# Optimization experiments

Hardware: AMD Instinct MI355X
Metric: run time of the kernel (lower is better)

Reference implementation:

```python
import jax, jax.numpy as jnp
import numpy as np

H, E, K = 1024, 8, 2  # hidden_size, num_experts, top_k
B, S = 2, 4096


def setup_inputs() -> dict:
    key = jax.random.key(0)
    ks = jax.random.split(key, 5)
    s = 1.0 / np.sqrt(H)
    return {
        "x": jax.random.normal(ks[0], (B, S, H), dtype=jnp.float32),
        "ln_scale": jnp.ones((H,), jnp.float32),
        "ln_bias": jnp.zeros((H,), jnp.float32),
        "w1": (jax.random.normal(ks[1], (H, H), jnp.float32) * s),
        "b1": jnp.zeros((H,), jnp.float32),
        "w2": (jax.random.normal(ks[2], (H, E), jnp.float32) * s),
        "b2": jnp.zeros((E,), jnp.float32),
        "We": (jax.random.normal(ks[3], (E, H, H), jnp.float32) * s),
        "be": jnp.zeros((E, H), jnp.float32),
    }


def _layernorm(x, scale, bias, eps=1e-5):
    m = jnp.mean(x, axis=-1, keepdims=True)
    v = jnp.var(x, axis=-1, keepdims=True)
    return (x - m) * jax.lax.rsqrt(v + eps) * scale + bias


def reference(x, ln_scale, ln_bias, w1, b1, w2, b2, We, be):
    b, s, h = x.shape
    # --- router (BaseRouter): LN -> MLP -> softmax -> top-k -> renorm ---
    xn = _layernorm(x, ln_scale, ln_bias)
    hmid = jax.nn.relu(xn @ w1 + b1)
    logits = hmid @ w2 + b2                      # [B,S,E]
    probs = jax.nn.softmax(logits, axis=-1)
    topk_p, topk_i = jax.lax.top_k(probs, K)     # [B,S,K]
    topk_p = topk_p / jnp.sum(topk_p, axis=-1, keepdims=True)
    # sparse combine weights [B,S,E]: renormalized top-k gate, 0 elsewhere
    cw = jnp.sum(topk_p[..., None] * jax.nn.one_hot(topk_i, E, dtype=x.dtype), axis=-2)
    # --- expert dispatch / weighted combine ---
    t = b * s
    xf = x.reshape(t, h)
    cwf = cw.reshape(t, E)
    ye = jnp.einsum('th,ehd->etd', xf, We) + be[:, None, :]   # [E,T,H]
    out = jnp.einsum('te,etd->td', cwf, ye).reshape(b, s, h)
    # --- aux load-balance loss ---
    mean_p = jnp.mean(probs, axis=(0, 1))        # [E]
    aux = jnp.sum(mean_p * jnp.log(mean_p * E + 1e-9))
    return out, aux
```

## Files before the change

kernel.cpp:

```cpp
#include <hip/hip_runtime.h>
#include <hip/hip_fp16.h>

#define H 1024
#define E 8
#define TT 8192

typedef __attribute__((ext_vector_type(8))) short bf16x8;
typedef __attribute__((ext_vector_type(4))) float f32x4;

__device__ __forceinline__ unsigned short f2bf(float f) {
  unsigned int u = __float_as_uint(f);
  u += 0x7fffu + ((u >> 16) & 1u);
  return (unsigned short)(u >> 16);
}

__device__ __forceinline__ int swz(int row, int c) {
  return (row << 5) | (((c ^ (row >> 1)) & 3) << 3);
}

__device__ __forceinline__ void gld16(void* lds, const void* g) {
  __builtin_amdgcn_global_load_lds((const __attribute__((address_space(1))) void*)g,
                                   (__attribute__((address_space(3))) void*)lds, 16, 0, 0);
}

__global__ __launch_bounds__(256) void k_pre(const float* __restrict__ w1, const float* __restrict__ lsc,
                                             const float* __restrict__ lbi, const float* __restrict__ x,
                                             unsigned short* __restrict__ w1h, unsigned short* __restrict__ w1l,
                                             float* __restrict__ part, float2* __restrict__ stats,
                                             unsigned short* __restrict__ xb, int* __restrict__ cnt,
                                             double* __restrict__ psum) {
  int blk = blockIdx.x;
  int t = threadIdx.x;
  if (blk < 1024) {
    __shared__ float tile[32][33];
    __shared__ float red[8][33];
    int kb = (blk & 31) << 5, nb = (blk >> 5) << 5;
    int cc = t & 31, rr = t >> 5;
    if (blk == 0 && t < E) { cnt[t] = 0; psum[t] = 0.0; }
#pragma unroll
    for (int r = 0; r < 4; ++r) {
      int k = kb + rr + (r << 3);
      tile[rr + (r << 3)][cc] = w1[(size_t)k * H + nb + cc];
    }
    __syncthreads();
    float pp = 0.f;
#pragma unroll
    for (int r = 0; r < 4; ++r) {
      int kk = rr + (r << 3);
      pp = fmaf(lbi[kb + kk], tile[kk][cc], pp);
    }
    red[rr][cc] = pp;
    float scale = lsc[kb + cc];
    __syncthreads();
    if (rr == 0) {
      float s = 0.f;
#pragma unroll
      for (int j = 0; j < 8; ++j) s += red[j][cc];
      part[(blk & 31) * H + nb + cc] = s;
    }
#pragma unroll
    for (int r = 0; r < 4; ++r) {
      int n = nb + rr + (r << 3);
      float v = tile[cc][rr + (r << 3)] * scale;
      unsigned short h = f2bf(v);
      float hv = __uint_as_float((unsigned)h << 16);
      unsigned short l = f2bf(v - hv);
      w1h[(size_t)n * H + kb + cc] = h;
      w1l[(size_t)n * H + kb + cc] = l;
    }
  } else {
    int tok = blk - 1024;
    const float4 v = *reinterpret_cast<const float4*>(&x[(size_t)tok * H + (t << 2)]);
    float s = v.x + v.y + v.z + v.w;
    float ss = v.x * v.x + v.y * v.y + v.z * v.z + v.w * v.w;
#pragma unroll
    for (int off = 32; off; off >>= 1) { s += __shfl_down(s, off); ss += __shfl_down(ss, off); }
    __shared__ float red2[4][2];
    int lane = t & 63, wv = t >> 6;
    if (lane == 0) { red2[wv][0] = s; red2[wv][1] = ss; }
    __syncthreads();
    float fs = red2[0][0] + red2[1][0] + red2[2][0] + red2[3][0];
    float fss = red2[0][1] + red2[1][1] + red2[2][1] + red2[3][1];
    float mean = fs * (1.0f / H);
    float var = fss * (1.0f / H) - mean * mean;
    float rstd = rsqrtf(var + 1e-5f);
    if (t == 0) stats[tok] = make_float2(mean, rstd);
    ushort4 ob;
    ob.x = f2bf(v.x); ob.y = f2bf(v.y); ob.z = f2bf(v.z); ob.w = f2bf(v.w);
    *reinterpret_cast<ushort4*>(&xb[(size_t)tok * H + (t << 2)]) = ob;
  }
}

__global__ __launch_bounds__(256) void k_router_mfma(
    const float* __restrict__ x, const float2* __restrict__ stats,
    const unsigned short* __restrict__ w1h, const unsigned short* __restrict__ w1l,
    const float* __restrict__ part, const float* __restrict__ b1, const float* __restrict__ w2,
    float* __restrict__ plog) {
  __shared__ __align__(16) short Ah[4096], Al[4096], Bh[4096], Bl[4096];
  __shared__ float2 st[128];
  int t = threadIdx.x;
  int bm = blockIdx.x << 7, bn = blockIdx.y << 7;
  if (t < 128) st[t] = stats[bm + t];
  __syncthreads();
  int arow = t >> 1, ac0 = (t & 1) << 1;
  int brow = t >> 2, bc = t & 3;
  float2 mr = st[arow];
  float rs = mr.y, mb = -mr.x * mr.y;
  const float* xsrc = &x[(size_t)(bm + arow) * H + (ac0 << 3)];
  const unsigned short* s1 = &w1h[(size_t)(bn + brow) * H + (bc << 3)];
  const unsigned short* s2 = &w1h[(size_t)(bn + brow + 64) * H + (bc << 3)];
  const unsigned short* s3 = &w1l[(size_t)(bn + brow) * H + (bc << 3)];
  const unsigned short* s4 = &w1l[(size_t)(bn + brow + 64) * H + (bc << 3)];
  float4 va0 = *(const float4*)(xsrc + 0), va1 = *(const float4*)(xsrc + 4);
  float4 va2 = *(const float4*)(xsrc + 8), va3 = *(const float4*)(xsrc + 12);
  int4 vb0 = *(const int4*)s1, vb1 = *(const int4*)s2, vb2 = *(const int4*)s3, vb3 = *(const int4*)s4;
  int lane = t & 63, wv = t >> 6;
  int wr = (wv >> 1) << 6, wc = (wv & 1) << 6;
  int l15 = lane & 15, lgp = lane >> 4;
  f32x4 acc[4][4];
#pragma unroll
  for (int i = 0; i < 4; ++i)
#pragma unroll
    for (int j = 0; j < 4; ++j) acc[i][j] = f32x4{0.f, 0.f, 0.f, 0.f};
  for (int kt = 0; kt < 32; ++kt) {
    float zz[16];
    zz[0] = fmaf(va0.x, rs, mb); zz[1] = fmaf(va0.y, rs, mb);
    zz[2] = fmaf(va0.z, rs, mb); zz[3] = fmaf(va0.w, rs, mb);
    zz[4] = fmaf(va1.x, rs, mb); zz[5] = fmaf(va1.y, rs, mb);
    zz[6] = fmaf(va1.z, rs, mb); zz[7] = fmaf(va1.w, rs, mb);
    zz[8] = fmaf(va2.x, rs, mb); zz[9] = fmaf(va2.y, rs, mb);
    zz[10] = fmaf(va2.z, rs, mb); zz[11] = fmaf(va2.w, rs, mb);
    zz[12] = fmaf(va3.x, rs, mb); zz[13] = fmaf(va3.y, rs, mb);
    zz[14] = fmaf(va3.z, rs, mb); zz[15] = fmaf(va3.w, rs, mb);
    unsigned hw[8], lw[8];
#pragma unroll
    for (int p = 0; p < 8; ++p) {
      unsigned ua = __float_as_uint(zz[2 * p]), ub = __float_as_uint(zz[2 * p + 1]);
      hw[p] = (ua >> 16) | (ub & 0xffff0000u);
      float la = zz[2 * p] - __uint_as_float(ua & 0xffff0000u);
      float lb = zz[2 * p + 1] - __uint_as_float(ub & 0xffff0000u);
      lw[p] = (__float_as_uint(la) >> 16) | (__float_as_uint(lb) & 0xffff0000u);
    }
    __syncthreads();
    *(int4*)&Ah[swz(arow, ac0)] = make_int4(hw[0], hw[1], hw[2], hw[3]);
    *(int4*)&Ah[swz(arow, ac0 + 1)] = make_int4(hw[4], hw[5], hw[6], hw[7]);
    *(int4*)&Al[swz(arow, ac0)] = make_int4(lw[0], lw[1], lw[2], lw[3]);
    *(int4*)&Al[swz(arow, ac0 + 1)] = make_int4(lw[4], lw[5], lw[6], lw[7]);
    *(int4*)&Bh[swz(brow, bc)] = vb0;
    *(int4*)&Bh[swz(brow + 64, bc)] = vb1;
    *(int4*)&Bl[swz(brow, bc)] = vb2;
    *(int4*)&Bl[swz(brow + 64, bc)] = vb3;
    __syncthreads();
    if (kt + 1 < 32) {
      xsrc += 32; s1 += 32; s2 += 32; s3 += 32; s4 += 32;
      va0 = *(const float4*)(xsrc + 0); va1 = *(const float4*)(xsrc + 4);
      va2 = *(const float4*)(xsrc + 8); va3 = *(const float4*)(xsrc + 12);
      vb0 = *(const int4*)s1; vb1 = *(const int4*)s2; vb2 = *(const int4*)s3; vb3 = *(const int4*)s4;
    }
    bf16x8 bh[4], bl[4];
#pragma unroll
    for (int j = 0; j < 4; ++j) {
      bh[j] = *(const bf16x8*)&Bh[swz(wc + (j << 4) + l15, lgp)];
      bl[j] = *(const bf16x8*)&Bl[swz(wc + (j << 4) + l15, lgp)];
    }
#pragma unroll
    for (int i = 0; i < 4; ++i) {
      bf16x8 ah = *(const bf16x8*)&Ah[swz(wr + (i << 4) + l15, lgp)];
      bf16x8 al = *(const bf16x8*)&Al[swz(wr + (i << 4) + l15, lgp)];
#pragma unroll
      for (int j = 0; j < 4; ++j) {
        acc[i][j] = __builtin_amdgcn_mfma_f32_16x16x32_bf16(ah, bh[j], acc[i][j], 0, 0, 0);
        acc[i][j] = __builtin_amdgcn_mfma_f32_16x16x32_bf16(ah, bl[j], acc[i][j], 0, 0, 0);
        acc[i][j] = __builtin_amdgcn_mfma_f32_16x16x32_bf16(al, bh[j], acc[i][j], 0, 0, 0);
      }
    }
  }
  float w2r[4][8], b1r[4];
#pragma unroll
  for (int j = 0; j < 4; ++j) {
    int col = bn + wc + (j << 4) + l15;
    float4 p0 = *(const float4*)&w2[(size_t)col * E];
    float4 p1 = *(const float4*)&w2[(size_t)col * E + 4];
    w2r[j][0] = p0.x; w2r[j][1] = p0.y; w2r[j][2] = p0.z; w2r[j][3] = p0.w;
    w2r[j][4] = p1.x; w2r[j][5] = p1.y; w2r[j][6] = p1.z; w2r[j][7] = p1.w;
    float s = b1[col];
    for (int jj = 0; jj < 32; ++jj) s += part[jj * H + col];
    b1r[j] = s;
  }
#pragma unroll
  for (int i = 0; i < 4; ++i)
#pragma unroll
    for (int j = 0; j < 4; ++j)
#pragma unroll
      for (int r = 0; r < 4; ++r) acc[i][j][r] = fmaxf(acc[i][j][r] + b1r[j], 0.f);
  int wh = wc >> 6;
  size_t pbase = ((size_t)(blockIdx.y * 2 + wh) * TT + bm) * E;
#pragma unroll
  for (int e = 0; e < E; ++e) {
    float se[4][4];
#pragma unroll
    for (int i = 0; i < 4; ++i)
#pragma unroll
      for (int r = 0; r < 4; ++r)
        se[i][r] = acc[i][0][r] * w2r[0][e] + acc[i][1][r] * w2r[1][e] +
                   acc[i][2][r] * w2r[2][e] + acc[i][3][r] * w2r[3][e];
#pragma unroll
    for (int off = 1; off < 16; off <<= 1)
#pragma unroll
      for (int i = 0; i < 4; ++i)
#pragma unroll
        for (int r = 0; r < 4; ++r) se[i][r] += __shfl_xor(se[i][r], off);
    if (l15 == 0) {
#pragma unroll
      for (int i = 0; i < 4; ++i)
#pragma unroll
        for (int r = 0; r < 4; ++r) {
          int row = wr + (i << 4) + (lgp << 2) + r;
          plog[pbase + (size_t)row * E + e] = se[i][r];
        }
    }
  }
}

__global__ __launch_bounds__(256) void k_top(const float* __restrict__ plog, const float* __restrict__ b2,
                                             int* __restrict__ topE, float* __restrict__ topW,
                                             int* __restrict__ listIdx, float* __restrict__ listW,
                                             int* __restrict__ cnt, double* __restrict__ psum) {
  int t = threadIdx.x, lane = t & 63;
  int tok = (blockIdx.x << 8) + t;
  float lg[E], p[E];
  float4 ba = *reinterpret_cast<const float4*>(b2);
  float4 bb = *reinterpret_cast<const float4*>(b2 + 4);
  lg[0] = ba.x; lg[1] = ba.y; lg[2] = ba.z; lg[3] = ba.w;
  lg[4] = bb.x; lg[5] = bb.y; lg[6] = bb.z; lg[7] = bb.w;
#pragma unroll
  for (int nb = 0; nb < 16; ++nb) {
    const float* pp = &plog[((size_t)nb * TT + tok) * E];
    float4 q0 = *reinterpret_cast<const float4*>(pp);
    float4 q1 = *reinterpret_cast<const float4*>(pp + 4);
    lg[0] += q0.x; lg[1] += q0.y; lg[2] += q0.z; lg[3] += q0.w;
    lg[4] += q1.x; lg[5] += q1.y; lg[6] += q1.z; lg[7] += q1.w;
  }
  float m = lg[0];
#pragma unroll
  for (int e = 1; e < E; ++e) m = fmaxf(m, lg[e]);
  float s = 0.f;
#pragma unroll
  for (int e = 0; e < E; ++e) { p[e] = __expf(lg[e] - m); s += p[e]; }
  float inv = 1.f / s;
#pragma unroll
  for (int e = 0; e < E; ++e) p[e] *= inv;
  {
    float ps[E];
#pragma unroll
    for (int e = 0; e < E; ++e) ps[e] = p[e];
#pragma unroll
    for (int off = 1; off < 64; off <<= 1)
#pragma unroll
      for (int e = 0; e < E; ++e) ps[e] += __shfl_xor(ps[e], off);
    if (lane == 0)
#pragma unroll
      for (int e = 0; e < E; ++e) atomicAdd(&psum[e], (double)ps[e]);
  }
  int e0 = 0;
#pragma unroll
  for (int e = 1; e < E; ++e) if (p[e] > p[e0]) e0 = e;
  int e1 = (e0 == 0) ? 1 : 0;
#pragma unroll
  for (int e = 0; e < E; ++e) if (e != e0 && p[e] > p[e1]) e1 = e;
  float rsw = 1.f / (p[e0] + p[e1]);
  float w0 = p[e0] * rsw, w1v = p[e1] * rsw;
  topE[tok << 1] = e0; topE[(tok << 1) + 1] = e1;
  topW[tok << 1] = w0; topW[(tok << 1) + 1] = w1v;
  unsigned long long lt = (1ull << lane) - 1ull;
#pragma unroll
  for (int e = 0; e < E; ++e) {
    unsigned long long m0 = __ballot(e0 == e);
    unsigned long long m1 = __ballot(e1 == e);
    int n0 = __popcll(m0), total = n0 + __popcll(m1);
    if (total == 0) continue;
    int leader = __ffsll(m0 | m1) - 1;
    int base = 0;
    if (lane == leader) base = atomicAdd(&cnt[e], total);
    base = __shfl(base, leader);
    if (e0 == e) {
      int pos = e * TT + base + __popcll(m0 & lt);
      listIdx[pos] = (tok << 1); listW[pos] = w0;
    }
    if (e1 == e) {
      int pos = e * TT + base + n0 + __popcll(m1 & lt);
      listIdx[pos] = (tok << 1) | 1; listW[pos] = w1v;
    }
  }
}

#define WL_SLOTS 2560
__global__ __launch_bounds__(256) void k_cast_we(const float* __restrict__ we, unsigned short* __restrict__ wet,
                                                 const int* __restrict__ cnt, int* __restrict__ workList) {
  __shared__ unsigned short tile[32][33];
  int e = blockIdx.z;
  int kb = blockIdx.x << 5, nb = blockIdx.y << 5;
  int t = threadIdx.x;
  if (blockIdx.x == 0 && blockIdx.y == 0 && blockIdx.z == 0) {
    for (int i = t; i < WL_SLOTS; i += 256) workList[i] = -1;
    __syncthreads();
    if (t < E) {
      int ee = t;
      int nbk = (cnt[ee] + 127) >> 7;
      int ov = 2048 + (ee << 6);
      int g = 0;
      for (int bx = 0; bx < nbk; ++bx) {
        for (int by = 0; by < 8; ++by) {
          int item = (ee << 12) | (bx << 4) | by;
          int slot = (g < 256) ? ((g << 3) + ee) : ov++;
          workList[slot] = item;
          ++g;
        }
      }
    }
    __syncthreads();
  }
  int cc = t & 31, rr = t >> 5;
  size_t base = (size_t)e * H * H;
#pragma unroll
  for (int r = 0; r < 4; ++r) {
    int k = kb + rr + (r << 3);
    tile[rr + (r << 3)][cc] = f2bf(we[base + (size_t)k * H + nb + cc]);
  }
  __syncthreads();
#pragma unroll
  for (int r = 0; r < 4; ++r) {
    int n = nb + rr + (r << 3);
    wet[base + (size_t)n * H + kb + cc] = tile[cc][rr + (r << 3)];
  }
}

__global__ __launch_bounds__(256) void k_expert_gemm(const unsigned short* __restrict__ xb,
                                                     const unsigned short* __restrict__ wet,
                                                     const int* __restrict__ listIdx, const float* __restrict__ listW,
                                                     const int* __restrict__ cnt, const int* __restrict__ workList,
                                                     unsigned short* __restrict__ ys) {
  int item = workList[blockIdx.x];
  if (item < 0) return;
  int e = item >> 12, bx = (item >> 4) & 255, by = item & 15;
  int c = cnt[e];
  int r0 = bx << 7, n0 = by << 7;
  __shared__ __align__(16) short A[2][4096], Bs[2][4096];
  __shared__ int gi[128];
  __shared__ float gw[128];
  int t = threadIdx.x;
  if (t < 128) {
    int rr = r0 + t;
    gi[t] = (rr < c) ? listIdx[e * TT + rr] : -1;
    gw[t] = (rr < c) ? listW[e * TT + rr] : 0.f;
  }
  __syncthreads();
  int w = t >> 6, lane = t & 63;
  int l15 = lane & 15, lgp = lane >> 4;
  int wr = (w >> 1) << 6, wc = (w & 1) << 6;
  int s0 = (w << 7) + lane, s1 = s0 + 64;
  int rA0 = s0 >> 2, cg0 = (s0 & 3) ^ ((rA0 >> 1) & 3);
  int rA1 = s1 >> 2, cg1 = (s1 & 3) ^ ((rA1 >> 1) & 3);
  int pk0 = gi[rA0], pk1 = gi[rA1];
  const unsigned short* srcA0 = xb + (size_t)((pk0 < 0) ? 0 : (pk0 >> 1)) * H + (cg0 << 3);
  const unsigned short* srcA1 = xb + (size_t)((pk1 < 0) ? 0 : (pk1 >> 1)) * H + (cg1 << 3);
  size_t wbase = (size_t)e * H * H;
  const unsigned short* srcB0 = wet + wbase + (size_t)(n0 + rA0) * H + (cg0 << 3);
  const unsigned short* srcB1 = wet + wbase + (size_t)(n0 + rA1) * H + (cg1 << 3);
  int d0 = (w << 10), d1 = d0 + 512;
  f32x4 acc[4][4];
#pragma unroll
  for (int i = 0; i < 4; ++i)
#pragma unroll
    for (int j = 0; j < 4; ++j) acc[i][j] = f32x4{0.f, 0.f, 0.f, 0.f};
  gld16(&A[0][d0], srcA0); gld16(&A[0][d1], srcA1);
  gld16(&Bs[0][d0], srcB0); gld16(&Bs[0][d1], srcB1);
#pragma unroll
  for (int kt = 0; kt < 32; ++kt) {
    const int cur = kt & 1, nxt = cur ^ 1;
    if (kt < 31) {
      const int ko = (kt + 1) << 5;
      gld16(&A[nxt][d0], srcA0 + ko); gld16(&A[nxt][d1], srcA1 + ko);
      gld16(&Bs[nxt][d0], srcB0 + ko); gld16(&Bs[nxt][d1], srcB1 + ko);
      asm volatile("s_waitcnt vmcnt(4)" ::: "memory");
    } else {
      asm volatile("s_waitcnt vmcnt(0)" ::: "memory");
    }
    __builtin_amdgcn_sched_barrier(0);
    __builtin_amdgcn_s_barrier();
    __builtin_amdgcn_sched_barrier(0);
    bf16x8 bq[4];
#pragma unroll
    for (int j = 0; j < 4; ++j) bq[j] = *(const bf16x8*)&Bs[cur][swz(wc + (j << 4) + l15, lgp)];
    bf16x8 aq[4];
#pragma unroll
    for (int i = 0; i < 4; ++i) aq[i] = *(const bf16x8*)&A[cur][swz(wr + (i << 4) + l15, lgp)];
    __builtin_amdgcn_s_setprio(1);
#pragma unroll
    for (int i = 0; i < 4; ++i)
#pragma unroll
      for (int j = 0; j < 4; ++j)
        acc[i][j] = __builtin_amdgcn_mfma_f32_16x16x32_bf16(aq[i], bq[j], acc[i][j], 0, 0, 0);
    __builtin_amdgcn_s_setprio(0);
    if (kt < 31) {
      __builtin_amdgcn_sched_barrier(0);
      __builtin_amdgcn_s_barrier();
    }
  }
#pragma unroll
  for (int i = 0; i < 4; ++i) {
#pragma unroll
    for (int r = 0; r < 4; ++r) {
      int row = wr + (i << 4) + (lgp << 2) + r;
      int pk = gi[row];
      if (pk < 0) continue;
      int tok = pk >> 1, slot = pk & 1;
      float wgt = gw[row];
      size_t ob = ((size_t)slot * TT + tok) * H + n0 + wc + l15;
#pragma unroll
      for (int j = 0; j < 4; ++j) ys[ob + (j << 4)] = __half_as_ushort(__float2half(wgt * acc[i][j][r]));
    }
  }
}

__global__ __launch_bounds__(256) void k_combine(const unsigned short* __restrict__ ys, const int* __restrict__ topE,
                                                 const float* __restrict__ topW, const float* __restrict__ be,
                                                 const double* __restrict__ psum, float* __restrict__ out) {
  int tok = blockIdx.x, t = threadIdx.x;
  if (tok == 0 && t == 0) {
    double a = 0.0;
    for (int e = 0; e < E; ++e) {
      double mp = psum[e] / (double)TT;
      a += mp * log(mp * (double)E + 1e-9);
    }
    out[(size_t)TT * H] = (float)a;
  }
  int e0 = topE[tok << 1], e1 = topE[(tok << 1) + 1];
  float w0 = topW[tok << 1], w1v = topW[(tok << 1) + 1];
  int h = t << 2;
  size_t base = (size_t)tok * H + h;
  ushort4 a = *reinterpret_cast<const ushort4*>(&ys[base]);
  ushort4 b = *reinterpret_cast<const ushort4*>(&ys[(size_t)TT * H + base]);
  float4 b0 = *reinterpret_cast<const float4*>(&be[e0 * H + h]);
  float4 b1v = *reinterpret_cast<const float4*>(&be[e1 * H + h]);
  float4 o;
  o.x = __half2float(__ushort_as_half(a.x)) + __half2float(__ushort_as_half(b.x)) + w0 * b0.x + w1v * b1v.x;
  o.y = __half2float(__ushort_as_half(a.y)) + __half2float(__ushort_as_half(b.y)) + w0 * b0.y + w1v * b1v.y;
  o.z = __half2float(__ushort_as_half(a.z)) + __half2float(__ushort_as_half(b.z)) + w0 * b0.z + w1v * b1v.z;
  o.w = __half2float(__ushort_as_half(a.w)) + __half2float(__ushort_as_half(b.w)) + w0 * b0.w + w1v * b1v.w;
  *reinterpret_cast<float4*>(&out[base]) = o;
}

extern "C" void kernel_launch(void* const* d_in, const int* in_sizes, int n_in, void* d_out, int out_size, void* d_ws,
                              size_t ws_size, hipStream_t stream) {
  const float* x = (const float*)d_in[0];
  const float* lsc = (const float*)d_in[1];
  const float* lbi = (const float*)d_in[2];
  const float* w1 = (const float*)d_in[3];
  const float* b1 = (const float*)d_in[4];
  const float* w2 = (const float*)d_in[5];
  const float* b2 = (const float*)d_in[6];
  const float* we = (const float*)d_in[7];
  const float* be = (const float*)d_in[8];
  float* out = (float*)d_out;
  char* ws = (char*)d_ws;

  char* p = ws;
  int* topE = (int*)p; p += TT * 2 * 4;
  float* topW = (float*)p; p += TT * 2 * 4;
  int* listIdx = (int*)p; p += E * TT * 4;
  float* listW = (float*)p; p += E * TT * 4;
  int* cnt = (int*)p; p += 256;
  double* psum = (double*)p; p += 2048;
  float* part = (float*)p; p += 32 * H * 4;
  int* workList = (int*)p; p += WL_SLOTS * 4;
  float2* stats = (float2*)p; p += TT * 8;
  unsigned short* xb = (unsigned short*)(ws + (2ull << 20));
  unsigned short* wet = (unsigned short*)(ws + (18ull << 20));
  unsigned short* w1h = (unsigned short*)(ws + (34ull << 20));
  unsigned short* w1l = (unsigned short*)(ws + (36ull << 20));
  float* plog = (float*)(ws + (38ull << 20));
  unsigned short* ys = (unsigned short*)(ws + (34ull << 20));

  k_pre<<<1024 + TT, 256, 0, stream>>>(w1, lsc, lbi, x, w1h, w1l, part, stats, xb, cnt, psum);
  k_router_mfma<<<dim3(TT / 128, H / 128), 256, 0, stream>>>(x, stats, w1h, w1l, part, b1, w2, plog);
  k_top<<<TT / 256, 256, 0, stream>>>(plog, b2, topE, topW, listIdx, listW, cnt, psum);
  k_cast_we<<<dim3(32, 32, E), 256, 0, stream>>>(we, wet, cnt, workList);
  k_expert_gemm<<<WL_SLOTS, 256, 0, stream>>>(xb, wet, listIdx, listW, cnt, workList, ys);
  k_combine<<<TT, 256, 0, stream>>>(ys, topE, topW, be, psum, out);
}
```

Baseline: 204.4 us.

## Fold expert weight cast into pre kernel and triple-buffer expert GEMM loads

Moves the fp32-to-bf16 transpose-cast of the expert weights out of its own kernel and into the k_pre launch as extra blocks, leaving a tiny single-block scheduling kernel to build the work list. This removes one large kernel's serialization and lets the cast share a launch with the LN stats and w1 prep work. The expert GEMM also switches from double to triple buffering in LDS, issuing loads two k-tiles ahead with one barrier per iteration instead of two. The cost is more shared memory per block, which may lower occupancy, and a larger pre kernel launch.

Result: slower. 209.9 us (+2.7%).

```diff
diff --git a/kernel.cpp b/kernel.cpp
--- a/kernel.cpp
+++ b/kernel.cpp
@@ -25,9 +25,10 @@
 
 __global__ __launch_bounds__(256) void k_pre(const float* __restrict__ w1, const float* __restrict__ lsc,
                                              const float* __restrict__ lbi, const float* __restrict__ x,
-                                             unsigned short* __restrict__ w1h, unsigned short* __restrict__ w1l,
-                                             float* __restrict__ part, float2* __restrict__ stats,
-                                             unsigned short* __restrict__ xb, int* __restrict__ cnt,
+                                             const float* __restrict__ we, unsigned short* __restrict__ w1h,
+                                             unsigned short* __restrict__ w1l, float* __restrict__ part,
+                                             float2* __restrict__ stats, unsigned short* __restrict__ xb,
+                                             unsigned short* __restrict__ wet, int* __restrict__ cnt,
                                              double* __restrict__ psum) {
   int blk = blockIdx.x;
   int t = threadIdx.x;
@@ -68,7 +69,7 @@
       w1h[(size_t)n * H + kb + cc] = h;
       w1l[(size_t)n * H + kb + cc] = l;
     }
-  } else {
+  } else if (blk < 9216) {
     int tok = blk - 1024;
     const float4 v = *reinterpret_cast<const float4*>(&x[(size_t)tok * H + (t << 2)]);
     float s = v.x + v.y + v.z + v.w;
@@ -88,6 +89,25 @@
     ushort4 ob;
     ob.x = f2bf(v.x); ob.y = f2bf(v.y); ob.z = f2bf(v.z); ob.w = f2bf(v.w);
     *reinterpret_cast<ushort4*>(&xb[(size_t)tok * H + (t << 2)]) = ob;
+  } else {
+    __shared__ unsigned short tile[32][33];
+    int idx = blk - 9216;
+    int e = idx >> 10;
+    int rem = idx & 1023;
+    int kb = (rem & 31) << 5, nb = (rem >> 5) << 5;
+    int cc = t & 31, rr = t >> 5;
+    size_t base = (size_t)e * H * H;
+#pragma unroll
+    for (int r = 0; r < 4; ++r) {
+      int k = kb + rr + (r << 3);
+      tile[rr + (r << 3)][cc] = f2bf(we[base + (size_t)k * H + nb + cc]);
+    }
+    __syncthreads();
+#pragma unroll
+    for (int r = 0; r < 4; ++r) {
+      int n = nb + rr + (r << 3);
+      wet[base + (size_t)n * H + kb + cc] = tile[cc][rr + (r << 3)];
+    }
   }
 }
 
@@ -295,43 +315,23 @@
 }
 
 #define WL_SLOTS 2560
-__global__ __launch_bounds__(256) void k_cast_we(const float* __restrict__ we, unsigned short* __restrict__ wet,
-                                                 const int* __restrict__ cnt, int* __restrict__ workList) {
-  __shared__ unsigned short tile[32][33];
-  int e = blockIdx.z;
-  int kb = blockIdx.x << 5, nb = blockIdx.y << 5;
+__global__ __launch_bounds__(256) void k_sched(const int* __restrict__ cnt, int* __restrict__ workList) {
   int t = threadIdx.x;
-  if (blockIdx.x == 0 && blockIdx.y == 0 && blockIdx.z == 0) {
-    for (int i = t; i < WL_SLOTS; i += 256) workList[i] = -1;
-    __syncthreads();
-    if (t < E) {
-      int ee = t;
-      int nbk = (cnt[ee] + 127) >> 7;
-      int ov = 2048 + (ee << 6);
-      int g = 0;
-      for (int bx = 0; bx < nbk; ++bx) {
-        for (int by = 0; by < 8; ++by) {
-          int item = (ee << 12) | (bx << 4) | by;
-          int slot = (g < 256) ? ((g << 3) + ee) : ov++;
-          workList[slot] = item;
-          ++g;
-        }
+  for (int i = t; i < WL_SLOTS; i += 256) workList[i] = -1;
+  __syncthreads();
+  if (t < E) {
+    int e = t;
+    int nb = (cnt[e] + 127) >> 7;
+    int ov = 2048 + (e << 6);
+    int g = 0;
+    for (int bx = 0; bx < nb; ++bx) {
+      for (int by = 0; by < 8; ++by) {
+        int item = (e << 12) | (bx << 4) | by;
+        int slot = (g < 256) ? ((g << 3) + e) : ov++;
+        workList[slot] = item;
+        ++g;
       }
     }
-    __syncthreads();
-  }
-  int cc = t & 31, rr = t >> 5;
-  size_t base = (size_t)e * H * H;
-#pragma unroll
-  for (int r = 0; r < 4; ++r) {
-    int k = kb + rr + (r << 3);
-    tile[rr + (r << 3)][cc] = f2bf(we[base + (size_t)k * H + nb + cc]);
-  }
-  __syncthreads();
-#pragma unroll
-  for (int r = 0; r < 4; ++r) {
-    int n = nb + rr + (r << 3);
-    wet[base + (size_t)n * H + kb + cc] = tile[cc][rr + (r << 3)];
   }
 }
 
@@ -345,7 +345,7 @@
   int e = item >> 12, bx = (item >> 4) & 255, by = item & 15;
   int c = cnt[e];
   int r0 = bx << 7, n0 = by << 7;
-  __shared__ __align__(16) short A[2][4096], Bs[2][4096];
+  __shared__ __align__(16) short A[3][4096], Bs[3][4096];
   __shared__ int gi[128];
   __shared__ float gw[128];
   int t = threadIdx.x;
@@ -373,15 +373,15 @@
   for (int i = 0; i < 4; ++i)
 #pragma unroll
     for (int j = 0; j < 4; ++j) acc[i][j] = f32x4{0.f, 0.f, 0.f, 0.f};
-  gld16(&A[0][d0], srcA0); gld16(&A[0][d1], srcA1);
-  gld16(&Bs[0][d0], srcB0); gld16(&Bs[0][d1], srcB1);
+#pragma unroll
+  for (int pt = 0; pt < 2; ++pt) {
+    const int ko = pt << 5;
+    gld16(&A[pt][d0], srcA0 + ko); gld16(&A[pt][d1], srcA1 + ko);
+    gld16(&Bs[pt][d0], srcB0 + ko); gld16(&Bs[pt][d1], srcB1 + ko);
+  }
 #pragma unroll
   for (int kt = 0; kt < 32; ++kt) {
-    const int cur = kt & 1, nxt = cur ^ 1;
-    if (kt < 31) {
-      const int ko = (kt + 1) << 5;
-      gld16(&A[nxt][d0], srcA0 + ko); gld16(&A[nxt][d1], srcA1 + ko);
-      gld16(&Bs[nxt][d0], srcB0 + ko); gld16(&Bs[nxt][d1], srcB1 + ko);
+    if (kt <= 30) {
       asm volatile("s_waitcnt vmcnt(4)" ::: "memory");
     } else {
       asm volatile("s_waitcnt vmcnt(0)" ::: "memory");
@@ -389,6 +389,12 @@
     __builtin_amdgcn_sched_barrier(0);
     __builtin_amdgcn_s_barrier();
     __builtin_amdgcn_sched_barrier(0);
+    if (kt <= 29) {
+      const int bnxt = (kt + 2) % 3, ko = (kt + 2) << 5;
+      gld16(&A[bnxt][d0], srcA0 + ko); gld16(&A[bnxt][d1], srcA1 + ko);
+      gld16(&Bs[bnxt][d0], srcB0 + ko); gld16(&Bs[bnxt][d1], srcB1 + ko);
+    }
+    const int cur = kt % 3;
     bf16x8 bq[4];
 #pragma unroll
     for (int j = 0; j < 4; ++j) bq[j] = *(const bf16x8*)&Bs[cur][swz(wc + (j << 4) + l15, lgp)];
@@ -402,10 +408,6 @@
       for (int j = 0; j < 4; ++j)
         acc[i][j] = __builtin_amdgcn_mfma_f32_16x16x32_bf16(aq[i], bq[j], acc[i][j], 0, 0, 0);
     __builtin_amdgcn_s_setprio(0);
-    if (kt < 31) {
-      __builtin_amdgcn_sched_barrier(0);
-      __builtin_amdgcn_s_barrier();
-    }
   }
 #pragma unroll
   for (int i = 0; i < 4; ++i) {
@@ -482,10 +484,10 @@
   float* plog = (float*)(ws + (38ull << 20));
   unsigned short* ys = (unsigned short*)(ws + (34ull << 20));
 
-  k_pre<<<1024 + TT, 256, 0, stream>>>(w1, lsc, lbi, x, w1h, w1l, part, stats, xb, cnt, psum);
+  k_pre<<<1024 + TT + 8192, 256, 0, stream>>>(w1, lsc, lbi, x, we, w1h, w1l, part, stats, xb, wet, cnt, psum);
   k_router_mfma<<<dim3(TT / 128, H / 128), 256, 0, stream>>>(x, stats, w1h, w1l, part, b1, w2, plog);
   k_top<<<TT / 256, 256, 0, stream>>>(plog, b2, topE, topW, listIdx, listW, cnt, psum);
-  k_cast_we<<<dim3(32, 32, E), 256, 0, stream>>>(we, wet, cnt, workList);
+  k_sched<<<1, 256, 0, stream>>>(cnt, workList);
   k_expert_gemm<<<WL_SLOTS, 256, 0, stream>>>(xb, wet, listIdx, listW, cnt, workList, ys);
   k_combine<<<TT, 256, 0, stream>>>(ys, topE, topW, be, psum, out);
 }
```
